# Kernel tuning notes

Hardware: AMD Instinct MI355X
Metric: run time of the kernel (lower is better)

## Reference

```python
import jax, jax.numpy as jnp
import numpy as np
import math

B, T, EMB = 2, 2048, 2048
HQ = HKV = 16
HD = EMB // HQ  # 128
MAX_SEQ = 2048


def _rope(x, cos, sin):
    # x: [b, t, h, d]; pairs are consecutive (view_as_complex on reshape(..., -1, 2))
    b, t, h, d = x.shape
    xp = x.astype(jnp.float32).reshape(b, t, h, d // 2, 2)
    xr, xi = xp[..., 0], xp[..., 1]
    c = cos[None, :, None, :]  # [1, t, 1, d/2]
    s = sin[None, :, None, :]
    or_ = xr * c - xi * s
    oi_ = xr * s + xi * c
    out = jnp.stack([or_, oi_], axis=-1).reshape(b, t, h, d)
    return out.astype(x.dtype)


def setup_inputs() -> dict:
    key = jax.random.key(0)
    ks = jax.random.split(key, 6)
    x = jax.random.normal(ks[0], (B, T, EMB), dtype=jnp.float32)
    # torch Linear weights: [out_features, in_features], y = x @ W.T
    sc = 1.0 / math.sqrt(EMB)
    wq = jax.random.normal(ks[1], (EMB, EMB), dtype=jnp.float32) * sc
    wk = jax.random.normal(ks[2], (EMB, EMB), dtype=jnp.float32) * sc
    wv = jax.random.normal(ks[3], (EMB, EMB), dtype=jnp.float32) * sc
    wo = jax.random.normal(ks[4], (EMB, EMB), dtype=jnp.float32) * sc
    # RoPE frequencies (llama-style), head_dim/2 angles per position
    inv_freq = 1.0 / (10000.0 ** (np.arange(0, HD, 2, dtype=np.float32) / HD))
    angles = np.arange(T, dtype=np.float32)[:, None] * inv_freq[None, :]  # [T, HD/2]
    freqs_cos = jnp.asarray(np.cos(angles))
    freqs_sin = jnp.asarray(np.sin(angles))
    k_cache = jnp.zeros((B, MAX_SEQ, HKV, HD), dtype=jnp.float32)
    v_cache = jnp.zeros((B, MAX_SEQ, HKV, HD), dtype=jnp.float32)
    return {"x": x, "wq": wq, "wk": wk, "wv": wv, "wo": wo,
            "k_cache": k_cache, "v_cache": v_cache,
            "freqs_cos": freqs_cos, "freqs_sin": freqs_sin, "start_pos": 0}


def reference(x, wq, wk, wv, wo, k_cache, v_cache, freqs_cos, freqs_sin, start_pos):
    b, t, c = x.shape
    xq = (x @ wq.T).reshape(b, t, HQ, HD)
    xk = (x @ wk.T).reshape(b, t, HKV, HD)
    xv = (x @ wv.T).reshape(b, t, HKV, HD)
    xq = _rope(xq, freqs_cos, freqs_sin)
    xk = _rope(xk, freqs_cos, freqs_sin)
    # KV-cache update at start_pos, then read prefix [0, start_pos+t)
    k_cache = jax.lax.dynamic_update_slice(k_cache, xk, (0, start_pos, 0, 0))
    v_cache = jax.lax.dynamic_update_slice(v_cache, xv, (0, start_pos, 0, 0))
    keys = k_cache[:, :start_pos + t]    # [b, s, hkv, d]
    values = v_cache[:, :start_pos + t]
    # n_rep = HQ // HKV = 1 -> repeat_kv is identity
    q = xq.transpose(0, 2, 1, 3)         # [b, h, t, d]
    k = keys.transpose(0, 2, 1, 3)       # [b, h, s, d]
    v = values.transpose(0, 2, 1, 3)
    scores = jnp.einsum('bhtd,bhsd->bhts', q, k) / math.sqrt(HD)
    scores = jax.nn.softmax(scores.astype(jnp.float32), axis=-1).astype(q.dtype)
    out = jnp.einsum('bhts,bhsd->bhtd', scores, v)
    out = out.transpose(0, 2, 1, 3).reshape(b, t, -1)
    return out @ wo.T
```

## Files before the change

kernel.cpp:

```cpp
#include <hip/hip_runtime.h>
#include <cstdint>

using u16 = unsigned short;
using short8 = __attribute__((ext_vector_type(8))) short;
using floatx4 = __attribute__((ext_vector_type(4))) float;

__device__ __forceinline__ u16 f2b(float f) {
    unsigned u = __float_as_uint(f);
    u = (u + 0x7fffu + ((u >> 16) & 1u)) >> 16;
    return (u16)u;
}
__device__ __forceinline__ u16 f2b_fast(float f) {
    return (u16)((__float_as_uint(f) + 0x8000u) >> 16);
}
__device__ __forceinline__ float b2f(unsigned v) {
    return __uint_as_float(v << 16);
}
__device__ __forceinline__ float fast_exp2(float f) {
#if __has_builtin(__builtin_amdgcn_exp2f)
    return __builtin_amdgcn_exp2f(f);
#else
    return exp2f(f);
#endif
}
__device__ __forceinline__ void gl_lds16(const u16* g, u16* l) {
    __builtin_amdgcn_global_load_lds(
        (const __attribute__((address_space(1))) void*)(const void*)g,
        (__attribute__((address_space(3))) void*)(void*)l, 16, 0, 0);
}

__global__ void cvt5_kernel(const float* __restrict__ x, const float* __restrict__ wq,
                            const float* __restrict__ wk, const float* __restrict__ wv,
                            const float* __restrict__ wo, u16* __restrict__ xb,
                            u16* __restrict__ wqkvb, u16* __restrict__ wob) {
    int i = blockIdx.x * 256 + threadIdx.x;
    const float* src;
    u16* dst;
    int off;
    if (i < 2097152)      { src = x;  dst = xb;             off = i; }
    else if (i < 3145728) { src = wq; dst = wqkvb;          off = i - 2097152; }
    else if (i < 4194304) { src = wk; dst = wqkvb + 4194304; off = i - 3145728; }
    else if (i < 5242880) { src = wv; dst = wqkvb + 8388608; off = i - 4194304; }
    else                  { src = wo; dst = wob;            off = i - 5242880; }
    float4 v = ((const float4*)src)[off];
    uint2 o;
    o.x = (unsigned)f2b(v.x) | ((unsigned)f2b(v.y) << 16);
    o.y = (unsigned)f2b(v.z) | ((unsigned)f2b(v.w) << 16);
    *(uint2*)&dst[off * 4] = o;
}

template <int OUT_F32>
__global__ void gemm_bt(const u16* __restrict__ A, const u16* __restrict__ B,
                        void* __restrict__ Cp, int M, int N, int K) {
    __shared__ u16 As[128 * 32];
    __shared__ u16 Bs[128 * 32];
    const int tid = threadIdx.x;
    const int lane = tid & 63, w = tid >> 6;
    const int wm = w & 1, wn = w >> 1;
    const int m0 = blockIdx.y * 128, n0 = blockIdx.x * 128;
    const int r = lane & 15, q = lane >> 4;
    const int sw = (q ^ ((r >> 1) & 3)) * 8;

    floatx4 acc[4][4] = {};

    for (int k0 = 0; k0 < K; k0 += 32) {
        __syncthreads();
#pragma unroll
        for (int i = 0; i < 2; i++) {
            int c = i * 256 + tid;
            int row = c >> 2, slot = c & 3;
            int sch = (slot ^ ((row >> 1) & 3)) * 8;
            gl_lds16(A + (size_t)(m0 + row) * K + k0 + sch, As + c * 8);
            gl_lds16(B + (size_t)(n0 + row) * K + k0 + sch, Bs + c * 8);
        }
        __syncthreads();
        short8 af[4], bf[4];
#pragma unroll
        for (int mi = 0; mi < 4; mi++)
            af[mi] = *(const short8*)&As[(wm * 64 + mi * 16 + r) * 32 + sw];
#pragma unroll
        for (int ni = 0; ni < 4; ni++)
            bf[ni] = *(const short8*)&Bs[(wn * 64 + ni * 16 + r) * 32 + sw];
#pragma unroll
        for (int mi = 0; mi < 4; mi++)
#pragma unroll
            for (int ni = 0; ni < 4; ni++)
                acc[mi][ni] = __builtin_amdgcn_mfma_f32_16x16x32_bf16(af[mi], bf[ni], acc[mi][ni], 0, 0, 0);
    }
#pragma unroll
    for (int mi = 0; mi < 4; mi++)
#pragma unroll
        for (int ni = 0; ni < 4; ni++)
#pragma unroll
            for (int rr = 0; rr < 4; rr++) {
                int row = m0 + wm * 64 + mi * 16 + q * 4 + rr;
                int col = n0 + wn * 64 + ni * 16 + r;
                if (OUT_F32)
                    ((float*)Cp)[(size_t)row * N + col] = acc[mi][ni][rr];
                else
                    ((u16*)Cp)[(size_t)row * N + col] = f2b(acc[mi][ni][rr]);
            }
}

__global__ void prep_kernel(u16* __restrict__ xqkv, const float* __restrict__ fc,
                            const float* __restrict__ fs, u16* __restrict__ vt) {
    if (blockIdx.x < 16384) {
        int tid = blockIdx.x * 256 + threadIdx.x;
        int d2 = tid & 63;
        int h = (tid >> 6) & 15;
        int t = (tid >> 10) & 2047;
        int b = tid >> 21;
        float c = fc[t * 64 + d2], s = fs[t * 64 + d2];
        int base = (b * 2048 + t) * 6144 + h * 128 + d2 * 2;
        unsigned uq = *(unsigned*)&xqkv[base];
        float xr = b2f(uq & 0xffffu), xi = b2f(uq >> 16);
        *(unsigned*)&xqkv[base] =
            (unsigned)f2b(xr * c - xi * s) | ((unsigned)f2b(xr * s + xi * c) << 16);
        unsigned uk = *(unsigned*)&xqkv[base + 2048];
        xr = b2f(uk & 0xffffu); xi = b2f(uk >> 16);
        *(unsigned*)&xqkv[base + 2048] =
            (unsigned)f2b(xr * c - xi * s) | ((unsigned)f2b(xr * s + xi * c) << 16);
    } else {
        __shared__ u16 Ts[64][72];
        int vb = blockIdx.x - 16384;
        int t0 = (vb & 31) * 64, d0 = ((vb >> 5) & 1) * 64, bh = vb >> 6;
        int b = bh >> 4, h = bh & 15;
#pragma unroll
        for (int i = 0; i < 2; i++) {
            int c = i * 256 + threadIdx.x;
            int tr = c >> 3, c8 = (c & 7) * 8;
            short8 v = *(const short8*)&xqkv[(size_t)(b * 2048 + t0 + tr) * 6144 + 4096 + h * 128 + d0 + c8];
#pragma unroll
            for (int j = 0; j < 8; j++) Ts[tr][c8 + j] = ((u16)v[j]);
        }
        __syncthreads();
#pragma unroll
        for (int i = 0; i < 2; i++) {
            int c = i * 256 + threadIdx.x;
            int dr = c >> 3, t8 = (c & 7) * 8;
            short8 v;
#pragma unroll
            for (int j = 0; j < 8; j++) v[j] = (short)Ts[t8 + j][dr];
            *(short8*)&vt[((size_t)(bh * 128 + d0 + dr)) * 2048 + t0 + t8] = v;
        }
    }
}

__global__ __launch_bounds__(256, 2) void flash_kernel(const u16* __restrict__ xqkv,
                                                       const u16* __restrict__ vt,
                                                       u16* __restrict__ ao) {
    __shared__ u16 smem[25600];
    u16* Ks = smem;
    u16* Vs = smem + 8192;
    const int tid = threadIdx.x;
    const int lane = tid & 63, w = tid >> 6;
    const int qg = lane >> 4, r16 = lane & 15;
    const int swz = (qg ^ ((r16 >> 1) & 3)) * 8;
    u16* QPw = smem + 16384 + w * 2304;
    const int bh = blockIdx.y, b = bh >> 4, h = bh & 15;
    const int t0 = blockIdx.x * 128 + w * 32;
    const float sl2e = 0.08838834764831845f * 1.4426950408889634f;

    short8 qreg[2][4];
#pragma unroll
    for (int tf = 0; tf < 2; tf++)
#pragma unroll
        for (int kc = 0; kc < 4; kc++) {
            short8 qv = *(const short8*)&xqkv[(size_t)(b * 2048 + t0 + tf * 16 + r16) * 6144 +
                                              h * 128 + kc * 32 + qg * 8];
#pragma unroll
            for (int j = 0; j < 8; j++)
                qv[j] = (short)f2b(b2f((u16)qv[j]) * sl2e);
            qreg[tf][kc] = qv;
        }

    floatx4 oacc[2][8] = {};
    float lsum[2][4] = {};

    for (int s0 = 0; s0 < 2048; s0 += 64) {
        __syncthreads();
#pragma unroll
        for (int i = 0; i < 4; i++) {
            int c = i * 256 + tid;
            int kc = c >> 8, cc = c & 255, sr = cc >> 2, slot = cc & 3;
            int sch = (slot ^ ((sr >> 1) & 3)) * 8;
            gl_lds16(xqkv + (size_t)(b * 2048 + s0 + sr) * 6144 + 2048 + h * 128 + kc * 32 + sch,
                     Ks + c * 8);
        }
#pragma unroll
        for (int i = 0; i < 4; i++) {
            int c = i * 256 + tid;
            int sc = c >> 9, cc = c & 511, d = cc >> 2, slot = cc & 3;
            int sch = (slot ^ ((d >> 1) & 3)) * 8;
            gl_lds16(vt + (size_t)(bh * 128 + d) * 2048 + s0 + sc * 32 + sch, Vs + c * 8);
        }
        __syncthreads();

        floatx4 sacc[2][4] = {};
#pragma unroll
        for (int kc = 0; kc < 4; kc++)
#pragma unroll
            for (int ni = 0; ni < 4; ni++) {
                short8 bfr = *(const short8*)&Ks[kc * 2048 + (ni * 16 + r16) * 32 + swz];
                sacc[0][ni] = __builtin_amdgcn_mfma_f32_16x16x32_bf16(qreg[0][kc], bfr, sacc[0][ni], 0, 0, 0);
                sacc[1][ni] = __builtin_amdgcn_mfma_f32_16x16x32_bf16(qreg[1][kc], bfr, sacc[1][ni], 0, 0, 0);
            }

#pragma unroll
        for (int tf = 0; tf < 2; tf++)
#pragma unroll
            for (int ni = 0; ni < 4; ni++)
#pragma unroll
                for (int r = 0; r < 4; r++) {
                    float p = fast_exp2(sacc[tf][ni][r]);
                    lsum[tf][r] += p;
                    QPw[(tf * 16 + qg * 4 + r) * 72 + ni * 16 + r16] = f2b_fast(p);
                }

#pragma unroll
        for (int sc = 0; sc < 2; sc++) {
            short8 p0 = *(const short8*)&QPw[(r16) * 72 + sc * 32 + qg * 8];
            short8 p1 = *(const short8*)&QPw[(16 + r16) * 72 + sc * 32 + qg * 8];
#pragma unroll
            for (int dt = 0; dt < 8; dt++) {
                short8 a = *(const short8*)&Vs[sc * 4096 + (dt * 16 + r16) * 32 + swz];
                oacc[0][dt] = __builtin_amdgcn_mfma_f32_16x16x32_bf16(a, p0, oacc[0][dt], 0, 0, 0);
                oacc[1][dt] = __builtin_amdgcn_mfma_f32_16x16x32_bf16(a, p1, oacc[1][dt], 0, 0, 0);
            }
        }
    }

#pragma unroll
    for (int mm = 1; mm <= 8; mm <<= 1)
#pragma unroll
        for (int tf = 0; tf < 2; tf++)
#pragma unroll
            for (int r = 0; r < 4; r++) lsum[tf][r] += __shfl_xor(lsum[tf][r], mm);

    int src = (r16 >> 2) << 4;
#pragma unroll
    for (int tf = 0; tf < 2; tf++) {
        float l0 = __shfl(lsum[tf][0], src), l1 = __shfl(lsum[tf][1], src);
        float l2 = __shfl(lsum[tf][2], src), l3 = __shfl(lsum[tf][3], src);
        float lsel = (r16 & 2) ? ((r16 & 1) ? l3 : l2) : ((r16 & 1) ? l1 : l0);
        float inv = 1.0f / lsel;
#pragma unroll
        for (int dt = 0; dt < 8; dt++)
#pragma unroll
            for (int r = 0; r < 4; r++)
                QPw[r16 * 136 + dt * 16 + qg * 4 + r] = f2b(oacc[tf][dt][r] * inv);
#pragma unroll
        for (int i = 0; i < 4; i++) {
            int c = i * 64 + lane;
            int rowt = c >> 4, c8 = (c & 15) * 8;
            short8 v = *(const short8*)&QPw[rowt * 136 + c8];
            *(short8*)&ao[(size_t)(b * 2048 + t0 + tf * 16 + rowt) * 2048 + h * 128 + c8] = v;
        }
    }
}

extern "C" void kernel_launch(void* const* d_in, const int* in_sizes, int n_in,
                              void* d_out, int out_size, void* d_ws, size_t ws_size,
                              hipStream_t stream) {
    const float* x = (const float*)d_in[0];
    const float* wq = (const float*)d_in[1];
    const float* wk = (const float*)d_in[2];
    const float* wv = (const float*)d_in[3];
    const float* wo = (const float*)d_in[4];
    const float* fcos = (const float*)d_in[7];
    const float* fsin = (const float*)d_in[8];

    char* ws = (char*)d_ws;
    u16* xb    = (u16*)(ws);
    u16* wqkvb = (u16*)(ws + 16777216);
    u16* wob   = (u16*)(ws + 41943040);
    u16* xqkv  = (u16*)(ws + 50331648);
    u16* vt    = (u16*)(ws + 100663296);
    u16* ao    = (u16*)(ws + 117440512);

    cvt5_kernel<<<24576, 256, 0, stream>>>(x, wq, wk, wv, wo, xb, wqkvb, wob);
    gemm_bt<0><<<dim3(48, 32), 256, 0, stream>>>(xb, wqkvb, xqkv, 4096, 6144, 2048);
    prep_kernel<<<18432, 256, 0, stream>>>(xqkv, fcos, fsin, vt);
    flash_kernel<<<dim3(16, 32), 256, 0, stream>>>(xqkv, vt, ao);
    gemm_bt<1><<<dim3(16, 32), 256, 0, stream>>>(ao, wob, (float*)d_out, 4096, 2048, 2048);
}
```

Baseline: 441.8 us.

## Fuse RoPE into QKV GEMM epilogue and widen GEMM K-tile to 64

Applies rotary embedding inside the QKV projection GEMM epilogue using a lane shuffle to fetch the pair partner, eliminating the separate RoPE pass over Q and K. The V transpose becomes its own kernel. The GEMM K tile doubles to 64 with an 8-way XOR swizzle, halving barrier count per K. This costs more LDS per block and adds cos/sin loads in the epilogue.

New measurement: 437.3 us. Within noise of the previous version (-1.0%).

```diff
diff --git a/kernel.cpp b/kernel.cpp
--- a/kernel.cpp
+++ b/kernel.cpp
@@ -49,44 +49,49 @@
     *(uint2*)&dst[off * 4] = o;
 }
 
-template <int OUT_F32>
+template <int OUT_F32, int DO_ROPE>
 __global__ void gemm_bt(const u16* __restrict__ A, const u16* __restrict__ B,
-                        void* __restrict__ Cp, int M, int N, int K) {
-    __shared__ u16 As[128 * 32];
-    __shared__ u16 Bs[128 * 32];
+                        void* __restrict__ Cp, const float* __restrict__ fc,
+                        const float* __restrict__ fs, int M, int N, int K) {
+    __shared__ u16 As[128 * 64];
+    __shared__ u16 Bs[128 * 64];
     const int tid = threadIdx.x;
     const int lane = tid & 63, w = tid >> 6;
     const int wm = w & 1, wn = w >> 1;
     const int m0 = blockIdx.y * 128, n0 = blockIdx.x * 128;
     const int r = lane & 15, q = lane >> 4;
-    const int sw = (q ^ ((r >> 1) & 3)) * 8;
 
     floatx4 acc[4][4] = {};
 
-    for (int k0 = 0; k0 < K; k0 += 32) {
-        __syncthreads();
-#pragma unroll
-        for (int i = 0; i < 2; i++) {
+    for (int k0 = 0; k0 < K; k0 += 64) {
+        __syncthreads();
+#pragma unroll
+        for (int i = 0; i < 4; i++) {
             int c = i * 256 + tid;
-            int row = c >> 2, slot = c & 3;
-            int sch = (slot ^ ((row >> 1) & 3)) * 8;
+            int row = c >> 3, slot = c & 7;
+            int sch = (slot ^ (row & 7)) * 8;
             gl_lds16(A + (size_t)(m0 + row) * K + k0 + sch, As + c * 8);
             gl_lds16(B + (size_t)(n0 + row) * K + k0 + sch, Bs + c * 8);
         }
         __syncthreads();
-        short8 af[4], bf[4];
-#pragma unroll
-        for (int mi = 0; mi < 4; mi++)
-            af[mi] = *(const short8*)&As[(wm * 64 + mi * 16 + r) * 32 + sw];
-#pragma unroll
-        for (int ni = 0; ni < 4; ni++)
-            bf[ni] = *(const short8*)&Bs[(wn * 64 + ni * 16 + r) * 32 + sw];
-#pragma unroll
-        for (int mi = 0; mi < 4; mi++)
+#pragma unroll
+        for (int ks = 0; ks < 2; ks++) {
+            const int sw = ((ks * 4 + q) ^ (r & 7)) * 8;
+            short8 af[4], bf[4];
+#pragma unroll
+            for (int mi = 0; mi < 4; mi++)
+                af[mi] = *(const short8*)&As[(wm * 64 + mi * 16 + r) * 64 + sw];
 #pragma unroll
             for (int ni = 0; ni < 4; ni++)
-                acc[mi][ni] = __builtin_amdgcn_mfma_f32_16x16x32_bf16(af[mi], bf[ni], acc[mi][ni], 0, 0, 0);
-    }
+                bf[ni] = *(const short8*)&Bs[(wn * 64 + ni * 16 + r) * 64 + sw];
+#pragma unroll
+            for (int mi = 0; mi < 4; mi++)
+#pragma unroll
+                for (int ni = 0; ni < 4; ni++)
+                    acc[mi][ni] = __builtin_amdgcn_mfma_f32_16x16x32_bf16(af[mi], bf[ni], acc[mi][ni], 0, 0, 0);
+        }
+    }
+    const bool rope = DO_ROPE && (n0 < 4096);
 #pragma unroll
     for (int mi = 0; mi < 4; mi++)
 #pragma unroll
@@ -95,54 +100,43 @@
             for (int rr = 0; rr < 4; rr++) {
                 int row = m0 + wm * 64 + mi * 16 + q * 4 + rr;
                 int col = n0 + wn * 64 + ni * 16 + r;
+                float val = acc[mi][ni][rr];
+                if (rope) {
+                    int t = row & 2047;
+                    int d2 = (col & 127) >> 1;
+                    float cv = fc[t * 64 + d2], sv = fs[t * 64 + d2];
+                    float partner = __shfl_xor(val, 1);
+                    val = (r & 1) ? (partner * sv + val * cv)
+                                  : (val * cv - partner * sv);
+                }
                 if (OUT_F32)
-                    ((float*)Cp)[(size_t)row * N + col] = acc[mi][ni][rr];
+                    ((float*)Cp)[(size_t)row * N + col] = val;
                 else
-                    ((u16*)Cp)[(size_t)row * N + col] = f2b(acc[mi][ni][rr]);
+                    ((u16*)Cp)[(size_t)row * N + col] = f2b(val);
             }
 }
 
-__global__ void prep_kernel(u16* __restrict__ xqkv, const float* __restrict__ fc,
-                            const float* __restrict__ fs, u16* __restrict__ vt) {
-    if (blockIdx.x < 16384) {
-        int tid = blockIdx.x * 256 + threadIdx.x;
-        int d2 = tid & 63;
-        int h = (tid >> 6) & 15;
-        int t = (tid >> 10) & 2047;
-        int b = tid >> 21;
-        float c = fc[t * 64 + d2], s = fs[t * 64 + d2];
-        int base = (b * 2048 + t) * 6144 + h * 128 + d2 * 2;
-        unsigned uq = *(unsigned*)&xqkv[base];
-        float xr = b2f(uq & 0xffffu), xi = b2f(uq >> 16);
-        *(unsigned*)&xqkv[base] =
-            (unsigned)f2b(xr * c - xi * s) | ((unsigned)f2b(xr * s + xi * c) << 16);
-        unsigned uk = *(unsigned*)&xqkv[base + 2048];
-        xr = b2f(uk & 0xffffu); xi = b2f(uk >> 16);
-        *(unsigned*)&xqkv[base + 2048] =
-            (unsigned)f2b(xr * c - xi * s) | ((unsigned)f2b(xr * s + xi * c) << 16);
-    } else {
-        __shared__ u16 Ts[64][72];
-        int vb = blockIdx.x - 16384;
-        int t0 = (vb & 31) * 64, d0 = ((vb >> 5) & 1) * 64, bh = vb >> 6;
-        int b = bh >> 4, h = bh & 15;
-#pragma unroll
-        for (int i = 0; i < 2; i++) {
-            int c = i * 256 + threadIdx.x;
-            int tr = c >> 3, c8 = (c & 7) * 8;
-            short8 v = *(const short8*)&xqkv[(size_t)(b * 2048 + t0 + tr) * 6144 + 4096 + h * 128 + d0 + c8];
-#pragma unroll
-            for (int j = 0; j < 8; j++) Ts[tr][c8 + j] = ((u16)v[j]);
-        }
-        __syncthreads();
-#pragma unroll
-        for (int i = 0; i < 2; i++) {
-            int c = i * 256 + threadIdx.x;
-            int dr = c >> 3, t8 = (c & 7) * 8;
-            short8 v;
-#pragma unroll
-            for (int j = 0; j < 8; j++) v[j] = (short)Ts[t8 + j][dr];
-            *(short8*)&vt[((size_t)(bh * 128 + d0 + dr)) * 2048 + t0 + t8] = v;
-        }
+__global__ void vtrans_kernel(const u16* __restrict__ xqkv, u16* __restrict__ vt) {
+    __shared__ u16 Ts[64][72];
+    int bh = blockIdx.z, d0 = blockIdx.y * 64, t0 = blockIdx.x * 64;
+    int b = bh >> 4, h = bh & 15;
+#pragma unroll
+    for (int i = 0; i < 2; i++) {
+        int c = i * 256 + threadIdx.x;
+        int tr = c >> 3, c8 = (c & 7) * 8;
+        short8 v = *(const short8*)&xqkv[(size_t)(b * 2048 + t0 + tr) * 6144 + 4096 + h * 128 + d0 + c8];
+#pragma unroll
+        for (int j = 0; j < 8; j++) Ts[tr][c8 + j] = ((u16)v[j]);
+    }
+    __syncthreads();
+#pragma unroll
+    for (int i = 0; i < 2; i++) {
+        int c = i * 256 + threadIdx.x;
+        int dr = c >> 3, t8 = (c & 7) * 8;
+        short8 v;
+#pragma unroll
+        for (int j = 0; j < 8; j++) v[j] = (short)Ts[t8 + j][dr];
+        *(short8*)&vt[((size_t)(bh * 128 + d0 + dr)) * 2048 + t0 + t8] = v;
     }
 }
 
@@ -279,8 +273,8 @@
     u16* ao    = (u16*)(ws + 117440512);
 
     cvt5_kernel<<<24576, 256, 0, stream>>>(x, wq, wk, wv, wo, xb, wqkvb, wob);
-    gemm_bt<0><<<dim3(48, 32), 256, 0, stream>>>(xb, wqkvb, xqkv, 4096, 6144, 2048);
-    prep_kernel<<<18432, 256, 0, stream>>>(xqkv, fcos, fsin, vt);
+    gemm_bt<0, 1><<<dim3(48, 32), 256, 0, stream>>>(xb, wqkvb, xqkv, fcos, fsin, 4096, 6144, 2048);
+    vtrans_kernel<<<dim3(32, 2, 32), 256, 0, stream>>>(xqkv, vt);
     flash_kernel<<<dim3(16, 32), 256, 0, stream>>>(xqkv, vt, ao);
-    gemm_bt<1><<<dim3(16, 32), 256, 0, stream>>>(ao, wob, (float*)d_out, 4096, 2048, 2048);
-}
+    gemm_bt<1, 0><<<dim3(16, 32), 256, 0, stream>>>(ao, wob, (float*)d_out, nullptr, nullptr, 4096, 2048, 2048);
+}
```
